# Optimization experiments

Measured on AMD Instinct MI355X. Metric: run time of the kernel, lower is better.

The kernel has to match this reference:

```python
import jax, jax.numpy as jnp
import numpy as np


def setup_inputs() -> dict:
    key = jax.random.key(0)
    k1, k2, k3 = jax.random.split(key, 3)
    B, T, H = 8, 2048, 2048
    original_hidden = jax.random.normal(k1, (B, T, H), dtype=jnp.float32)
    dag_hidden = jax.random.normal(k2, (B, T, H), dtype=jnp.float32)
    # nn.Linear(2H, 1): weight (1, 2H) -> stored transposed as (2H, 1)
    W_gate = jax.random.normal(k3, (2 * H, 1), dtype=jnp.float32) / np.sqrt(2 * H)
    b_gate = jnp.zeros((1,), dtype=jnp.float32)
    return {"original_hidden": original_hidden, "dag_hidden": dag_hidden,
            "W_gate": W_gate, "b_gate": b_gate}


def reference(original_hidden, dag_hidden, W_gate, b_gate):
    # gate = sigmoid(concat([orig, dag], -1) @ W + b), computed for all (B,T) at once
    H = original_hidden.shape[-1]
    # Split W to avoid materializing the concatenated (B,T,2H) tensor
    W_o, W_d = W_gate[:H], W_gate[H:]  # each (H, 1)
    logits = (jnp.einsum('bth,ho->bto', original_hidden, W_o)
              + jnp.einsum('bth,ho->bto', dag_hidden, W_d) + b_gate)  # (B,T,1)
    gate = jax.nn.sigmoid(logits)
    mixed_hidden = original_hidden + gate * (dag_hidden - original_hidden)
    # gate_values: per-timestep (B,1) gates in original; return stacked (B,T,1)
    gate_values = jax.lax.stop_gradient(gate)
    return (mixed_hidden, gate_values)
```

## Files before the change

kernel.cpp:

```cpp
#include <hip/hip_runtime.h>


constexpr int H_DIM   = 2048;
constexpr int BLOCK   = 256;
constexpr int VEC_PER = H_DIM / 4 / BLOCK;

__global__ __launch_bounds__(BLOCK) void dagmixer_fused(
    const float* __restrict__ orig,
    const float* __restrict__ dag,
    const float* __restrict__ Wg,
    const float* __restrict__ bg,
    float* __restrict__ mixed,
    float* __restrict__ gate_out)
{
    const int row  = blockIdx.x;
    const int t    = threadIdx.x;
    const long long base = (long long)row * H_DIM;

    const float4* o4  = reinterpret_cast<const float4*>(orig + base);
    const float4* d4  = reinterpret_cast<const float4*>(dag + base);
    const float4* wo4 = reinterpret_cast<const float4*>(Wg);
    const float4* wd4 = reinterpret_cast<const float4*>(Wg + H_DIM);

    float4 o[VEC_PER], d[VEC_PER];
    float partial = 0.0f;

#pragma unroll
    for (int i = 0; i < VEC_PER; ++i) {
        const int idx = t + i * BLOCK;
        o[i] = o4[idx];
        d[i] = d4[idx];
        const float4 wo = wo4[idx];
        const float4 wd = wd4[idx];
        partial += o[i].x * wo.x + o[i].y * wo.y + o[i].z * wo.z + o[i].w * wo.w;
        partial += d[i].x * wd.x + d[i].y * wd.y + d[i].z * wd.z + d[i].w * wd.w;
    }

#pragma unroll
    for (int off = 32; off > 0; off >>= 1)
        partial += __shfl_down(partial, off, 64);

    __shared__ float wsum[BLOCK / 64];
    const int wave = t >> 6;
    const int lane = t & 63;
    if (lane == 0) wsum[wave] = partial;
    __syncthreads();

    float logit = wsum[0] + wsum[1] + wsum[2] + wsum[3] + bg[0];
    const float gate = 1.0f / (1.0f + __expf(-logit));

    float4* m4 = reinterpret_cast<float4*>(mixed + base);
#pragma unroll
    for (int i = 0; i < VEC_PER; ++i) {
        const int idx = t + i * BLOCK;
        float4 m;
        m.x = o[i].x + gate * (d[i].x - o[i].x);
        m.y = o[i].y + gate * (d[i].y - o[i].y);
        m.z = o[i].z + gate * (d[i].z - o[i].z);
        m.w = o[i].w + gate * (d[i].w - o[i].w);
        m4[idx] = m;
    }

    if (t == 0) gate_out[row] = gate;
}

extern "C" void kernel_launch(void* const* d_in, const int* in_sizes, int n_in,
                              void* d_out, int out_size, void* d_ws, size_t ws_size,
                              hipStream_t stream) {
    const float* orig = (const float*)d_in[0];
    const float* dag  = (const float*)d_in[1];
    const float* Wg   = (const float*)d_in[2];
    const float* bg   = (const float*)d_in[3];

    const int total = in_sizes[0];
    const int rows  = total / H_DIM;

    float* mixed    = (float*)d_out;
    float* gate_out = (float*)d_out + (long long)total;

    dagmixer_fused<<<rows, BLOCK, 0, stream>>>(orig, dag, Wg, bg, mixed, gate_out);
}
```

Before: 304.4 us.

## Map one row per wave with persistent grid and register-cached gate weights

```diff
diff --git a/kernel.cpp b/kernel.cpp
--- a/kernel.cpp
+++ b/kernel.cpp
@@ -1,67 +1,75 @@
 #include <hip/hip_runtime.h>
 
 
-constexpr int H_DIM   = 2048;
-constexpr int BLOCK   = 256;
-constexpr int VEC_PER = H_DIM / 4 / BLOCK;
+constexpr int H_DIM  = 2048;
+constexpr int BLOCK  = 256;
+constexpr int F4_ROW = H_DIM / 4;
+constexpr int F4_PER = F4_ROW / 64;
 
-__global__ __launch_bounds__(BLOCK) void dagmixer_fused(
+__global__ __launch_bounds__(BLOCK, 3) void dagmixer_wave(
     const float* __restrict__ orig,
     const float* __restrict__ dag,
     const float* __restrict__ Wg,
     const float* __restrict__ bg,
     float* __restrict__ mixed,
-    float* __restrict__ gate_out)
+    float* __restrict__ gate_out,
+    int rows)
 {
-    const int row  = blockIdx.x;
-    const int t    = threadIdx.x;
-    const long long base = (long long)row * H_DIM;
+    const int lane     = threadIdx.x & 63;
+    const int wave_id  = (blockIdx.x * (BLOCK / 64)) + (threadIdx.x >> 6);
+    const int n_waves  = gridDim.x * (BLOCK / 64);
 
-    const float4* o4  = reinterpret_cast<const float4*>(orig + base);
-    const float4* d4  = reinterpret_cast<const float4*>(dag + base);
+    const float bias = bg[0];
+
     const float4* wo4 = reinterpret_cast<const float4*>(Wg);
     const float4* wd4 = reinterpret_cast<const float4*>(Wg + H_DIM);
+    float4 wo[F4_PER], wd[F4_PER];
+#pragma unroll
+    for (int k = 0; k < F4_PER; ++k) {
+        wo[k] = wo4[lane + k * 64];
+        wd[k] = wd4[lane + k * 64];
+    }
 
-    float4 o[VEC_PER], d[VEC_PER];
-    float partial = 0.0f;
+    for (int row = wave_id; row < rows; row += n_waves) {
+        const long long base4 = (long long)row * F4_ROW;
+        const float4* o4 = reinterpret_cast<const float4*>(orig) + base4;
+        const float4* d4 = reinterpret_cast<const float4*>(dag)  + base4;
+
+        float4 o[F4_PER], d[F4_PER];
+#pragma unroll
+        for (int k = 0; k < F4_PER; ++k) {
+            o[k] = o4[lane + k * 64];
+            d[k] = d4[lane + k * 64];
+        }
+
+        float partial = 0.0f;
+#pragma unroll
+        for (int k = 0; k < F4_PER; ++k) {
+            partial += o[k].x * wo[k].x + o[k].y * wo[k].y
+                     + o[k].z * wo[k].z + o[k].w * wo[k].w;
+            partial += d[k].x * wd[k].x + d[k].y * wd[k].y
+                     + d[k].z * wd[k].z + d[k].w * wd[k].w;
+        }
 
 #pragma unroll
-    for (int i = 0; i < VEC_PER; ++i) {
-        const int idx = t + i * BLOCK;
-        o[i] = o4[idx];
-        d[i] = d4[idx];
-        const float4 wo = wo4[idx];
-        const float4 wd = wd4[idx];
-        partial += o[i].x * wo.x + o[i].y * wo.y + o[i].z * wo.z + o[i].w * wo.w;
-        partial += d[i].x * wd.x + d[i].y * wd.y + d[i].z * wd.z + d[i].w * wd.w;
+        for (int m = 32; m > 0; m >>= 1)
+            partial += __shfl_xor(partial, m, 64);
+
+        const float gate = 1.0f / (1.0f + __expf(-(partial + bias)));
+
+        float4* m4 = reinterpret_cast<float4*>(mixed) + base4;
+#pragma unroll
+        for (int k = 0; k < F4_PER; ++k) {
+            float4 m;
+            m.x = fmaf(gate, d[k].x - o[k].x, o[k].x);
+            m.y = fmaf(gate, d[k].y - o[k].y, o[k].y);
+            m.z = fmaf(gate, d[k].z - o[k].z, o[k].z);
+            m.w = fmaf(gate, d[k].w - o[k].w, o[k].w);
+            m4[lane + k * 64] = m;
+        }
+
+        if (lane == 0) gate_out[row] = gate;
     }
-
-#pragma unroll
-    for (int off = 32; off > 0; off >>= 1)
-        partial += __shfl_down(partial, off, 64);
-
-    __shared__ float wsum[BLOCK / 64];
-    const int wave = t >> 6;
-    const int lane = t & 63;
-    if (lane == 0) wsum[wave] = partial;
-    __syncthreads();
-
-    float logit = wsum[0] + wsum[1] + wsum[2] + wsum[3] + bg[0];
-    const float gate = 1.0f / (1.0f + __expf(-logit));
-
-    float4* m4 = reinterpret_cast<float4*>(mixed + base);
-#pragma unroll
-    for (int i = 0; i < VEC_PER; ++i) {
-        const int idx = t + i * BLOCK;
-        float4 m;
-        m.x = o[i].x + gate * (d[i].x - o[i].x);
-        m.y = o[i].y + gate * (d[i].y - o[i].y);
-        m.z = o[i].z + gate * (d[i].z - o[i].z);
-        m.w = o[i].w + gate * (d[i].w - o[i].w);
-        m4[idx] = m;
-    }
-
-    if (t == 0) gate_out[row] = gate;
 }
 
 extern "C" void kernel_launch(void* const* d_in, const int* in_sizes, int n_in,
@@ -78,5 +86,7 @@
     float* mixed    = (float*)d_out;
     float* gate_out = (float*)d_out + (long long)total;
 
-    dagmixer_fused<<<rows, BLOCK, 0, stream>>>(orig, dag, Wg, bg, mixed, gate_out);
+    const int nblocks = 1024;
+    dagmixer_wave<<<nblocks, BLOCK, 0, stream>>>(orig, dag, Wg, bg,
+                                                 mixed, gate_out, rows);
 }
```

Result: slower. 311.1 us (+2.2%).
